# Optimization experiments

Hardware: AMD Instinct MI355X
Metric: run time of the kernel (lower is better)

Reference implementation:

```python
import jax, jax.numpy as jnp
import numpy as np

PS = 4            # phase-shift steps per direction
GC = 8            # gray-code bits per direction
BG_THR = 0.05     # background/modulation threshold
WAVELENGTH = 16.0 # fringe wavelength in pixels
PI = jnp.pi
H, W = 2048, 2448


def _phase_sums(imgs):
    # imgs: [N, H, W] N-step phase-shift images with shifts 2*pi*i/N
    n = imgs.shape[0]
    delta = 2.0 * PI * jnp.arange(n, dtype=imgs.dtype) / n
    s = jnp.einsum('n,nhw->hw', jnp.sin(delta), imgs)
    c = jnp.einsum('n,nhw->hw', jnp.cos(delta), imgs)
    return s, c


def _background(imgs):
    s, c = _phase_sums(imgs)
    return (2.0 / imgs.shape[0]) * jnp.sqrt(s * s + c * c)


def _phase(imgs):
    s, c = _phase_sums(imgs)
    return -jnp.arctan2(s, c)  # in [-pi, pi]


def _unwrap(ps, gc_imgs, threshold, ratio):
    # gray-code binarize against per-pixel threshold
    gray = gc_imgs > threshold                       # [GC, H, W] bool
    # sequential XOR decode: gray[i] ^= gray[i-1]  ==  cumulative XOR
    gray = jax.lax.associative_scan(jnp.logical_xor, gray, axis=0)
    gi = gray.astype(jnp.int32)
    dec_k1 = jnp.sum(gi[:-1] * ratio[1:, None, None], axis=0)   # [H, W]
    dec_v2 = jnp.sum(gi * ratio[:, None, None], axis=0)
    dec_k2 = (dec_v2 + 1) // 2
    m1 = (ps <= PI / 2)
    m3 = (ps >= 3 * PI / 2)
    m2 = jnp.logical_and(ps > PI / 2, ps < 3 * PI / 2)
    ps = (ps
          + (2 * PI) * dec_k2 * m1
          + (2 * PI) * dec_k1 * m2
          + ((2 * PI) * dec_k2 - 2 * PI) * m3)
    return ps


def setup_inputs() -> dict:
    key = jax.random.key(0)
    images = jax.random.uniform(key, (2 * PS + 2 * GC, H, W), dtype=jnp.float32)
    return {"images": images}


def reference(images):
    ps_imgs = images[:2 * PS]
    col_bg = _background(ps_imgs[:PS])
    row_bg = _background(ps_imgs[PS:])
    mask = jnp.logical_or(col_bg > BG_THR, row_bg > BG_THR).astype(images.dtype)
    threshold = jnp.mean(ps_imgs, axis=0)            # [H, W]

    ps_col = _phase(ps_imgs[:PS])
    ps_col = jnp.where(ps_col < 0, ps_col + 2 * PI, ps_col)
    ps_row = _phase(ps_imgs[PS:])
    ps_row = jnp.where(ps_row < 0, ps_row + 2 * PI, ps_row)

    gc = images[2 * PS:]
    ratio = jnp.asarray(2 ** np.arange(GC - 1, -1, -1), dtype=jnp.int32)

    ps_col = _unwrap(ps_col, gc[:GC], threshold, ratio)
    ps_row = _unwrap(ps_row, gc[GC:], threshold, ratio)

    scale = WAVELENGTH / (2 * PI)
    col = (ps_col * mask * scale)[..., None]         # [H, W, 1]
    row = (ps_row * mask * scale)[..., None]
    return jnp.concatenate([col, row], axis=2)       # [H, W, 2]
```

## Files before the change

### kernel.cpp

```cpp
#include <hip/hip_runtime.h>
#include <math.h>

#define H_ 2048
#define W_ 2448
#define HW (H_*W_)
#define HW4 (HW/4)

typedef float f4 __attribute__((ext_vector_type(4)));

#define SIN2_C  (-8.7422777e-08f)
#define COS1_C  (-4.3711388e-08f)
#define COS3_C  ( 1.1924881e-08f)
#define TWO_PI_F   6.2831854820251465f
#define PI_HALF_F  1.5707963705062866f
#define PI3HALF_F  4.7123889923095703f
#define SCALE_F    2.5464790894703254f
#define BG_THR_F   0.05f

__global__ __launch_bounds__(256)
void cg_kernel(const float* __restrict__ img, f4* __restrict__ out4) {
    const int t = blockIdx.x * 256 + threadIdx.x;
    const f4* in4 = (const f4*)img;

    f4 p[8];
#pragma unroll
    for (int i = 0; i < 8; ++i)
        p[i] = __builtin_nontemporal_load(&in4[(size_t)i * HW4 + t]);
    f4 g[16];
#pragma unroll
    for (int i = 0; i < 16; ++i)
        g[i] = __builtin_nontemporal_load(&in4[(size_t)(8 + i) * HW4 + t]);

    float col[4], row[4];
#pragma unroll
    for (int j = 0; j < 4; ++j) {
        const float i0 = p[0][j], i1 = p[1][j], i2 = p[2][j], i3 = p[3][j];
        const float i4 = p[4][j], i5 = p[5][j], i6 = p[6][j], i7 = p[7][j];

        float sc = __fsub_rn(__fadd_rn(i1, __fmul_rn(SIN2_C, i2)), i3);
        float cc = __fadd_rn(__fsub_rn(__fadd_rn(i0, __fmul_rn(COS1_C, i1)), i2),
                             __fmul_rn(COS3_C, i3));
        float sr = __fsub_rn(__fadd_rn(i5, __fmul_rn(SIN2_C, i6)), i7);
        float cr = __fadd_rn(__fsub_rn(__fadd_rn(i4, __fmul_rn(COS1_C, i5)), i6),
                             __fmul_rn(COS3_C, i7));

        float bgc = __fmul_rn(0.5f, __fsqrt_rn(__fadd_rn(__fmul_rn(sc, sc), __fmul_rn(cc, cc))));
        float bgr = __fmul_rn(0.5f, __fsqrt_rn(__fadd_rn(__fmul_rn(sr, sr), __fmul_rn(cr, cr))));
        float msk = (bgc > BG_THR_F || bgr > BG_THR_F) ? 1.0f : 0.0f;

        float thr = __fmul_rn(0.125f,
            __fadd_rn(__fadd_rn(__fadd_rn(i0, i1), __fadd_rn(i2, i3)),
                      __fadd_rn(__fadd_rn(i4, i5), __fadd_rn(i6, i7))));

        float psc = -atan2f(sc, cc);
        if (psc < 0.0f) psc = __fadd_rn(psc, TWO_PI_F);
        float psr = -atan2f(sr, cr);
        if (psr < 0.0f) psr = __fadd_rn(psr, TWO_PI_F);

        int cumc = 0, v2c = 0, k1c = 0;
        int cumr = 0, v2r = 0, k1r = 0;
#pragma unroll
        for (int i = 0; i < 8; ++i) {
            cumc ^= (g[i][j]     > thr) ? 1 : 0;
            cumr ^= (g[8 + i][j] > thr) ? 1 : 0;
            v2c += cumc << (7 - i);
            v2r += cumr << (7 - i);
            if (i < 7) { k1c += cumc << (6 - i); k1r += cumr << (6 - i); }
        }
        int k2c = (v2c + 1) >> 1;
        int k2r = (v2r + 1) >> 1;

        float ac;
        if (psc <= PI_HALF_F)      ac = __fmul_rn(TWO_PI_F, (float)k2c);
        else if (psc < PI3HALF_F)  ac = __fmul_rn(TWO_PI_F, (float)k1c);
        else                       ac = __fsub_rn(__fmul_rn(TWO_PI_F, (float)k2c), TWO_PI_F);
        float ar;
        if (psr <= PI_HALF_F)      ar = __fmul_rn(TWO_PI_F, (float)k2r);
        else if (psr < PI3HALF_F)  ar = __fmul_rn(TWO_PI_F, (float)k1r);
        else                       ar = __fsub_rn(__fmul_rn(TWO_PI_F, (float)k2r), TWO_PI_F);

        psc = __fadd_rn(psc, ac);
        psr = __fadd_rn(psr, ar);

        col[j] = __fmul_rn(__fmul_rn(psc, msk), SCALE_F);
        row[j] = __fmul_rn(__fmul_rn(psr, msk), SCALE_F);
    }

    f4 o0 = {col[0], row[0], col[1], row[1]};
    f4 o1 = {col[2], row[2], col[3], row[3]};
    __builtin_nontemporal_store(o0, &out4[(size_t)2 * t]);
    __builtin_nontemporal_store(o1, &out4[(size_t)2 * t + 1]);
}

extern "C" void kernel_launch(void* const* d_in, const int* in_sizes, int n_in,
                              void* d_out, int out_size, void* d_ws, size_t ws_size,
                              hipStream_t stream) {
    const float* img = (const float*)d_in[0];
    f4* out = (f4*)d_out;
    dim3 grid(HW4 / 256), block(256);
    hipLaunchKernelGGL(cg_kernel, grid, block, 0, stream, img, out);
}
```

Before: 594.4 us.

## Stream planes with double-buffered loads and 4x work per thread

Each thread now handles four float4 pixel groups and walks through the 24 input planes in order with two alternating load buffers, accumulating the phase sums, the threshold and packed gray-code bits as each plane arrives. The gray decode becomes a bitwise prefix-XOR on the packed bits. The grid shrinks fourfold. This aims to overlap loads with computation and cut register holding of all planes, but it raises the per-thread accumulator state and lowers the number of waves available to hide memory latency.

```diff
diff --git a/kernel.cpp b/kernel.cpp
--- a/kernel.cpp
+++ b/kernel.cpp
@@ -17,79 +17,132 @@
 #define SCALE_F    2.5464790894703254f
 #define BG_THR_F   0.05f
 
+
 __global__ __launch_bounds__(256)
 void cg_kernel(const float* __restrict__ img, f4* __restrict__ out4) {
-    const int t = blockIdx.x * 256 + threadIdx.x;
     const f4* in4 = (const f4*)img;
+    const size_t base = (size_t)blockIdx.x * 1024 + threadIdx.x;
 
-    f4 p[8];
-#pragma unroll
-    for (int i = 0; i < 8; ++i)
-        p[i] = __builtin_nontemporal_load(&in4[(size_t)i * HW4 + t]);
-    f4 g[16];
-#pragma unroll
-    for (int i = 0; i < 16; ++i)
-        g[i] = __builtin_nontemporal_load(&in4[(size_t)(8 + i) * HW4 + t]);
+    f4 A[4], B[4];
 
-    float col[4], row[4];
-#pragma unroll
-    for (int j = 0; j < 4; ++j) {
-        const float i0 = p[0][j], i1 = p[1][j], i2 = p[2][j], i3 = p[3][j];
-        const float i4 = p[4][j], i5 = p[5][j], i6 = p[6][j], i7 = p[7][j];
+#define LOADP(dst, p) \
+    _Pragma("unroll") \
+    for (int k = 0; k < 4; ++k) \
+        dst[k] = __builtin_nontemporal_load(&in4[(size_t)(p) * HW4 + base + (size_t)(k) * 256]);
 
-        float sc = __fsub_rn(__fadd_rn(i1, __fmul_rn(SIN2_C, i2)), i3);
-        float cc = __fadd_rn(__fsub_rn(__fadd_rn(i0, __fmul_rn(COS1_C, i1)), i2),
-                             __fmul_rn(COS3_C, i3));
-        float sr = __fsub_rn(__fadd_rn(i5, __fmul_rn(SIN2_C, i6)), i7);
-        float cr = __fadd_rn(__fsub_rn(__fadd_rn(i4, __fmul_rn(COS1_C, i5)), i6),
-                             __fmul_rn(COS3_C, i7));
+#define FORALL \
+    _Pragma("unroll") for (int k = 0; k < 4; ++k) \
+    _Pragma("unroll") for (int j = 0; j < 4; ++j)
 
-        float bgc = __fmul_rn(0.5f, __fsqrt_rn(__fadd_rn(__fmul_rn(sc, sc), __fmul_rn(cc, cc))));
-        float bgr = __fmul_rn(0.5f, __fsqrt_rn(__fadd_rn(__fmul_rn(sr, sr), __fmul_rn(cr, cr))));
-        float msk = (bgc > BG_THR_F || bgr > BG_THR_F) ? 1.0f : 0.0f;
+    float sc[4][4], cc[4][4], sr[4][4], cr[4][4];
+    float pair[4][4], s0123[4][4], thr[4][4];
 
-        float thr = __fmul_rn(0.125f,
-            __fadd_rn(__fadd_rn(__fadd_rn(i0, i1), __fadd_rn(i2, i3)),
-                      __fadd_rn(__fadd_rn(i4, i5), __fadd_rn(i6, i7))));
+#define P0(t) FORALL { float v = t[k][j]; cc[k][j] = v; pair[k][j] = v; }
+#define P1(t) FORALL { float v = t[k][j]; sc[k][j] = v; \
+    cc[k][j] = __fadd_rn(cc[k][j], __fmul_rn(COS1_C, v)); \
+    s0123[k][j] = __fadd_rn(pair[k][j], v); }
+#define P2(t) FORALL { float v = t[k][j]; \
+    sc[k][j] = __fadd_rn(sc[k][j], __fmul_rn(SIN2_C, v)); \
+    cc[k][j] = __fsub_rn(cc[k][j], v); pair[k][j] = v; }
+#define P3(t) FORALL { float v = t[k][j]; \
+    sc[k][j] = __fsub_rn(sc[k][j], v); \
+    cc[k][j] = __fadd_rn(cc[k][j], __fmul_rn(COS3_C, v)); \
+    s0123[k][j] = __fadd_rn(s0123[k][j], __fadd_rn(pair[k][j], v)); }
+#define P4(t) FORALL { float v = t[k][j]; cr[k][j] = v; pair[k][j] = v; }
+#define P5(t) FORALL { float v = t[k][j]; sr[k][j] = v; \
+    cr[k][j] = __fadd_rn(cr[k][j], __fmul_rn(COS1_C, v)); \
+    thr[k][j] = __fadd_rn(pair[k][j], v); }
+#define P6(t) FORALL { float v = t[k][j]; \
+    sr[k][j] = __fadd_rn(sr[k][j], __fmul_rn(SIN2_C, v)); \
+    cr[k][j] = __fsub_rn(cr[k][j], v); pair[k][j] = v; }
+#define P7(t) FORALL { float v = t[k][j]; \
+    sr[k][j] = __fsub_rn(sr[k][j], v); \
+    cr[k][j] = __fadd_rn(cr[k][j], __fmul_rn(COS3_C, v)); \
+    float s4567 = __fadd_rn(thr[k][j], __fadd_rn(pair[k][j], v)); \
+    thr[k][j] = __fmul_rn(0.125f, __fadd_rn(s0123[k][j], s4567)); }
 
-        float psc = -atan2f(sc, cc);
-        if (psc < 0.0f) psc = __fadd_rn(psc, TWO_PI_F);
-        float psr = -atan2f(sr, cr);
-        if (psr < 0.0f) psr = __fadd_rn(psr, TWO_PI_F);
+#define GCB(t, bit) FORALL { R[k][j] |= (t[k][j] > thr[k][j]) ? (1 << (bit)) : 0; }
 
-        int cumc = 0, v2c = 0, k1c = 0;
-        int cumr = 0, v2r = 0, k1r = 0;
-#pragma unroll
-        for (int i = 0; i < 8; ++i) {
-            cumc ^= (g[i][j]     > thr) ? 1 : 0;
-            cumr ^= (g[8 + i][j] > thr) ? 1 : 0;
-            v2c += cumc << (7 - i);
-            v2r += cumr << (7 - i);
-            if (i < 7) { k1c += cumc << (6 - i); k1r += cumr << (6 - i); }
-        }
-        int k2c = (v2c + 1) >> 1;
-        int k2r = (v2r + 1) >> 1;
+    LOADP(A, 0);
+    LOADP(B, 1);  P0(A);
+    LOADP(A, 2);  P1(B);
+    LOADP(B, 3);  P2(A);
+    LOADP(A, 4);  P3(B);
+    LOADP(B, 5);  P4(A);
+    LOADP(A, 6);  P5(B);
+    LOADP(B, 7);  P6(A);
+    LOADP(A, 8);  P7(B);
+    LOADP(B, 9);
 
-        float ac;
-        if (psc <= PI_HALF_F)      ac = __fmul_rn(TWO_PI_F, (float)k2c);
-        else if (psc < PI3HALF_F)  ac = __fmul_rn(TWO_PI_F, (float)k1c);
-        else                       ac = __fsub_rn(__fmul_rn(TWO_PI_F, (float)k2c), TWO_PI_F);
-        float ar;
-        if (psr <= PI_HALF_F)      ar = __fmul_rn(TWO_PI_F, (float)k2r);
-        else if (psr < PI3HALF_F)  ar = __fmul_rn(TWO_PI_F, (float)k1r);
-        else                       ar = __fsub_rn(__fmul_rn(TWO_PI_F, (float)k2r), TWO_PI_F);
-
-        psc = __fadd_rn(psc, ac);
-        psr = __fadd_rn(psr, ar);
-
-        col[j] = __fmul_rn(__fmul_rn(psc, msk), SCALE_F);
-        row[j] = __fmul_rn(__fmul_rn(psr, msk), SCALE_F);
+    float psc[4][4], psr[4][4], msk[4][4];
+    int R[4][4];
+    FORALL {
+        float scv = sc[k][j], ccv = cc[k][j], srv = sr[k][j], crv = cr[k][j];
+        float bgc = __fmul_rn(0.5f, __fsqrt_rn(__fadd_rn(__fmul_rn(scv, scv), __fmul_rn(ccv, ccv))));
+        float bgr = __fmul_rn(0.5f, __fsqrt_rn(__fadd_rn(__fmul_rn(srv, srv), __fmul_rn(crv, crv))));
+        msk[k][j] = (bgc > BG_THR_F || bgr > BG_THR_F) ? 1.0f : 0.0f;
+        float a = -atan2f(scv, ccv);
+        if (a < 0.0f) a = __fadd_rn(a, TWO_PI_F);
+        psc[k][j] = a;
+        float b = -atan2f(srv, crv);
+        if (b < 0.0f) b = __fadd_rn(b, TWO_PI_F);
+        psr[k][j] = b;
+        R[k][j] = 0;
     }
 
-    f4 o0 = {col[0], row[0], col[1], row[1]};
-    f4 o1 = {col[2], row[2], col[3], row[3]};
-    __builtin_nontemporal_store(o0, &out4[(size_t)2 * t]);
-    __builtin_nontemporal_store(o1, &out4[(size_t)2 * t + 1]);
+    GCB(A, 7);
+    LOADP(A, 10); GCB(B, 6);
+    LOADP(B, 11); GCB(A, 5);
+    LOADP(A, 12); GCB(B, 4);
+    LOADP(B, 13); GCB(A, 3);
+    LOADP(A, 14); GCB(B, 2);
+    LOADP(B, 15); GCB(A, 1);
+    LOADP(A, 16); GCB(B, 0);
+    LOADP(B, 17); GCB(A, 15);
+    LOADP(A, 18); GCB(B, 14);
+    LOADP(B, 19); GCB(A, 13);
+    LOADP(A, 20); GCB(B, 12);
+    LOADP(B, 21); GCB(A, 11);
+    LOADP(A, 22); GCB(B, 10);
+    LOADP(B, 23); GCB(A, 9);
+    GCB(B, 8);
+
+#pragma unroll
+    for (int k = 0; k < 4; ++k) {
+        float co[4], ro[4];
+#pragma unroll
+        for (int j = 0; j < 4; ++j) {
+            int Rv = R[k][j];
+            int vc = Rv & 0xFF;
+            vc ^= vc >> 1; vc ^= vc >> 2; vc ^= vc >> 4;
+            int vr = (Rv >> 8) & 0xFF;
+            vr ^= vr >> 1; vr ^= vr >> 2; vr ^= vr >> 4;
+            int k1c = vc >> 1, k2c = (vc + 1) >> 1;
+            int k1r = vr >> 1, k2r = (vr + 1) >> 1;
+
+            float a = psc[k][j];
+            float ac;
+            if (a <= PI_HALF_F)      ac = __fmul_rn(TWO_PI_F, (float)k2c);
+            else if (a < PI3HALF_F)  ac = __fmul_rn(TWO_PI_F, (float)k1c);
+            else                     ac = __fsub_rn(__fmul_rn(TWO_PI_F, (float)k2c), TWO_PI_F);
+            float b = psr[k][j];
+            float ar;
+            if (b <= PI_HALF_F)      ar = __fmul_rn(TWO_PI_F, (float)k2r);
+            else if (b < PI3HALF_F)  ar = __fmul_rn(TWO_PI_F, (float)k1r);
+            else                     ar = __fsub_rn(__fmul_rn(TWO_PI_F, (float)k2r), TWO_PI_F);
+
+            a = __fadd_rn(a, ac);
+            b = __fadd_rn(b, ar);
+            float m = msk[k][j];
+            co[j] = __fmul_rn(__fmul_rn(a, m), SCALE_F);
+            ro[j] = __fmul_rn(__fmul_rn(b, m), SCALE_F);
+        }
+        size_t q = base + (size_t)k * 256;
+        f4 o0 = {co[0], ro[0], co[1], ro[1]};
+        f4 o1 = {co[2], ro[2], co[3], ro[3]};
+        __builtin_nontemporal_store(o0, &out4[2 * q]);
+        __builtin_nontemporal_store(o1, &out4[2 * q + 1]);
+    }
 }
 
 extern "C" void kernel_launch(void* const* d_in, const int* in_sizes, int n_in,
@@ -97,6 +150,6 @@
                               hipStream_t stream) {
     const float* img = (const float*)d_in[0];
     f4* out = (f4*)d_out;
-    dim3 grid(HW4 / 256), block(256);
+    dim3 grid(HW4 / 1024), block(256);
     hipLaunchKernelGGL(cg_kernel, grid, block, 0, stream, img, out);
 }
```

After: 620.4 us. +4.4%, slower.
